# Optimization experiments

Hardware: AMD Instinct MI355X
Metric: run time of the kernel (lower is better)

Reference implementation:

```python
import jax, jax.numpy as jnp
import numpy as np

B, N, M, D = 64, 197, 65, 768


def setup_inputs() -> dict:
    key = jax.random.key(0)
    k1, k2, k3 = jax.random.split(key, 3)
    image = jax.random.normal(k1, (B, N, D), dtype=jnp.float32)
    text = jax.random.normal(k2, (B, M, D), dtype=jnp.float32)
    pm = jax.random.randint(k3, (B, M), 0, 2).astype(jnp.int32)
    pm = pm.at[:, :2].set(0)  # CLS + first real token always valid
    logit_scale = jnp.ones((), dtype=jnp.float32)
    return {"image": image, "text": text, "padding_masks": pm, "logit_scale": logit_scale}


def _ce_with_diag_labels(logits):
    # F.cross_entropy(logits, arange(B)): mean of -log_softmax diag
    return -jnp.mean(jnp.diagonal(jax.nn.log_softmax(logits, axis=-1)))


def reference(image, text, padding_masks, logit_scale):
    # include_cls_token=False: original computes full [B,B,N,M] then slices
    # [:, :, 1:, 1:]; we compute the sliced tokens directly (same math).
    img = image[:, 1:, :]                   # [B, N-1, D]
    txt = text[:, 1:, :]                    # [B, M-1, D]
    pm = padding_masks[:, 1:].astype(bool)  # [B, M-1] True = padded

    # sim[i,j,n,m] = logit_scale * <img_i,n , txt_j,m>
    sim = logit_scale * jnp.einsum('ind,jmd->ijnm', img, txt)  # [B,B,N-1,M-1]

    # Original masks with NaN along mask of batch-row i (broadcast over j,n).
    # logits_per_image: nan_to_num(-inf) -> max over m -> mean over n
    sim_img = jnp.where(pm[:, None, None, :], -jnp.inf, sim)
    logits_per_image = jnp.mean(jnp.max(sim_img, axis=3), axis=2)  # [B,B]

    # logits_per_text: max over n (NaN cols stay NaN) -> nanmean over m.
    # Equivalent masked mean over valid m (mask constant along n).
    max_n = jnp.max(sim, axis=2)                         # [B,B,M-1]
    valid = ~pm                                          # [B,M-1]
    cnt = jnp.sum(valid, axis=1).astype(sim.dtype)       # [B]
    logits_per_text = jnp.sum(
        jnp.where(valid[:, None, :], max_n, 0.0), axis=2
    ) / cnt[:, None]                                     # [B,B]

    loss = 0.5 * (_ce_with_diag_labels(logits_per_image)
                  + _ce_with_diag_labels(logits_per_text))
    targets = jnp.arange(logits_per_image.shape[0], dtype=jnp.int32)
    return loss, logits_per_image, logits_per_text, targets
```

## Files before the change

### kernel.cpp

```cpp
#include <hip/hip_runtime.h>

typedef _Float16 half8 __attribute__((ext_vector_type(8)));
typedef float floatx4 __attribute__((ext_vector_type(4)));
typedef float float4v __attribute__((ext_vector_type(4)));

#define AUNITS (64 * 13 * 24 * 64)
#define TUNITS (64 * 4 * 24 * 64)
#define A_HALFS ((size_t)AUNITS * 8)
#define BJ_HALFS (24 * 4 * 64 * 8)
#define AI_HALFS (13 * 24 * 512)

__device__ __forceinline__ void gl_lds16(const _Float16* g, _Float16* l) {
  __builtin_amdgcn_global_load_lds(
      (const __attribute__((address_space(1))) unsigned int*)g,
      (__attribute__((address_space(3))) unsigned int*)l, 16, 0, 0);
}

__global__ __launch_bounds__(256) void repack(const float* __restrict__ img,
                                              const float* __restrict__ txt,
                                              _Float16* __restrict__ Apk,
                                              _Float16* __restrict__ Bpk) {
  int gid = blockIdx.x * 256 + threadIdx.x;
  const float* src;
  _Float16* dst;
  if (gid < AUNITS) {
    int l = gid & 63, g = gid >> 6;
    int s = g % 24; g /= 24;
    int tau = g % 13; int i = g / 13;
    int n = tau * 16 + (l & 15); if (n > 195) n = 195;
    src = img + (size_t)i * 197 * 768 + (size_t)(n + 1) * 768 + s * 32 + (l >> 4) * 8;
    dst = Apk + (size_t)gid * 8;
  } else {
    int u = gid - AUNITS;
    int l = u & 63, g = u >> 6;
    int ct = g & 3; g >>= 2;
    int s = g % 24; int j = g / 24;
    int m = ct * 16 + (l & 15);
    src = txt + (size_t)j * 65 * 768 + (size_t)(m + 1) * 768 + s * 32 + (l >> 4) * 8;
    dst = Bpk + (size_t)u * 8;
  }
  float4v v0 = *(const float4v*)src;
  float4v v1 = *(const float4v*)(src + 4);
  half8 h;
  h[0] = (_Float16)v0[0]; h[1] = (_Float16)v0[1]; h[2] = (_Float16)v0[2]; h[3] = (_Float16)v0[3];
  h[4] = (_Float16)v1[0]; h[5] = (_Float16)v1[1]; h[6] = (_Float16)v1[2]; h[7] = (_Float16)v1[3];
  *(half8*)dst = h;
}

__global__ __launch_bounds__(256, 4) void sim_kernel(const _Float16* __restrict__ Apk,
                                                     const _Float16* __restrict__ Bpk,
                                                     const int* __restrict__ pm,
                                                     const float* __restrict__ ls,
                                                     float* __restrict__ lpi,
                                                     float* __restrict__ lpt) {
  __shared__ _Float16 Bsh[16384];

  const int j = blockIdx.x, i = blockIdx.y;
  const int tid = threadIdx.x;
  const int wave = tid >> 6, lane = tid & 63;
  const int r16 = lane & 15;
  const int lane8 = lane * 8;

  const _Float16* Ai = Apk + (size_t)i * AI_HALFS;
  const _Float16* pA[4];
  pA[0] = Ai + (size_t)(wave)     * 24 * 512 + lane8;
  pA[1] = Ai + (size_t)(wave + 4) * 24 * 512 + lane8;
  pA[2] = Ai + (size_t)(wave + 8) * 24 * 512 + lane8;
  pA[3] = Ai + (size_t)12         * 24 * 512 + lane8;
  const _Float16* Bg = Bpk + (size_t)j * BJ_HALFS;

  auto stage = [&](int cc) {
    const int buf = cc & 1;
#pragma unroll
    for (int r4 = 0; r4 < 4; ++r4) {
      int rr = wave * 4 + r4;
      gl_lds16(Bg + (size_t)(4 * cc) * 2048 + rr * 512 + lane8,
               Bsh + buf * 8192 + rr * 512);
    }
  };

  stage(0);
  __builtin_amdgcn_sched_barrier(0);
  half8 af[4];
#pragma unroll
  for (int t = 0; t < 4; ++t) af[t] = *(const half8*)(pA[t]);
  __builtin_amdgcn_sched_barrier(0);
  asm volatile("s_waitcnt vmcnt(4)" ::: "memory");
  __builtin_amdgcn_s_barrier();
  __builtin_amdgcn_sched_barrier(0);

  floatx4 acc[3][4];
  floatx4 acc12 = (floatx4){0.f, 0.f, 0.f, 0.f};
#pragma unroll
  for (int t = 0; t < 3; ++t)
#pragma unroll
    for (int cc = 0; cc < 4; ++cc)
      acc[t][cc] = (floatx4){0.f, 0.f, 0.f, 0.f};

#pragma unroll
  for (int c = 0; c < 6; ++c) {
#pragma unroll
    for (int sc = 0; sc < 4; ++sc) {
      const int s = c * 4 + sc;

      if (sc == 0 && c > 0) {
        asm volatile("s_waitcnt vmcnt(16)" ::: "memory");
        __builtin_amdgcn_s_barrier();
        __builtin_amdgcn_sched_barrier(0);
      }

      const int base = (c & 1) * 8192 + sc * 2048 + lane8;
      half8 b[4];
#pragma unroll
      for (int cc = 0; cc < 4; ++cc) {
        int ct = (wave + cc) & 3;
        b[cc] = *(const half8*)(Bsh + base + ct * 512);
      }

      if (sc == 0 && c < 5) {
        stage(c + 1);
        __builtin_amdgcn_sched_barrier(0);
      }

      __builtin_amdgcn_s_setprio(1);
#pragma unroll
      for (int cc = 0; cc < 4; ++cc) {
        acc[0][cc] = __builtin_amdgcn_mfma_f32_16x16x32_f16(af[0], b[cc], acc[0][cc], 0, 0, 0);
        acc[1][cc] = __builtin_amdgcn_mfma_f32_16x16x32_f16(af[1], b[cc], acc[1][cc], 0, 0, 0);
        acc[2][cc] = __builtin_amdgcn_mfma_f32_16x16x32_f16(af[2], b[cc], acc[2][cc], 0, 0, 0);
      }
      acc12 = __builtin_amdgcn_mfma_f32_16x16x32_f16(af[3], b[0], acc12, 0, 0, 0);
      __builtin_amdgcn_s_setprio(0);

      if (s < 23) {
#pragma unroll
        for (int t = 0; t < 4; ++t) af[t] = *(const half8*)(pA[t] + (s + 1) * 512);
      }
      __builtin_amdgcn_sched_barrier(0);
    }
  }

  const float sgl = ls[0];
  bool msk[4];
  int colc[4];
#pragma unroll
  for (int cc = 0; cc < 4; ++cc) {
    colc[cc] = ((wave + cc) & 3) * 16 + r16;
    msk[cc] = pm[i * 65 + 1 + colc[cc]] != 0;
  }

  float rowsum = 0.f;
  float cmv[4];
#pragma unroll
  for (int t = 0; t < 3; ++t) {
#pragma unroll
    for (int r = 0; r < 4; ++r) {
      float rm = -__builtin_inff();
#pragma unroll
      for (int cc = 0; cc < 4; ++cc) {
        float v = acc[t][cc][r] * sgl;
        rm = fmaxf(rm, msk[cc] ? -__builtin_inff() : v);
      }
#pragma unroll
      for (int off = 1; off < 16; off <<= 1)
        rm = fmaxf(rm, __shfl_xor(rm, off, 64));
      rowsum += rm;
    }
  }
#pragma unroll
  for (int off = 1; off < 64; off <<= 1) rowsum += __shfl_xor(rowsum, off, 64);

#pragma unroll
  for (int cc = 0; cc < 4; ++cc) {
    float cm = -__builtin_inff();
#pragma unroll
    for (int t = 0; t < 3; ++t)
#pragma unroll
      for (int r = 0; r < 4; ++r)
        cm = fmaxf(cm, acc[t][cc][r] * sgl);
    cm = fmaxf(cm, __shfl_xor(cm, 16, 64));
    cm = fmaxf(cm, __shfl_xor(cm, 32, 64));
    cmv[cc] = cm;
  }

  __syncthreads();
  float* colmaxS = (float*)Bsh;
  float* t12S    = (float*)Bsh + 256;
  float* wsumS   = (float*)Bsh + 512;

  if (lane == 0) wsumS[wave] = rowsum;
  if (lane < 16) {
#pragma unroll
    for (int cc = 0; cc < 4; ++cc) colmaxS[wave * 64 + colc[cc]] = cmv[cc];
#pragma unroll
    for (int r = 0; r < 4; ++r) t12S[r * 64 + wave * 16 + r16] = acc12[r] * sgl;
  }
  __syncthreads();

  if (tid < 64) {
    const int col = lane;
    bool valid = pm[i * 65 + 1 + col] == 0;
    float t0 = t12S[col], t1 = t12S[64 + col], t2 = t12S[128 + col], t3 = t12S[192 + col];
    float v = fmaxf(fmaxf(colmaxS[col], colmaxS[64 + col]),
                    fmaxf(colmaxS[128 + col], colmaxS[192 + col]));
    v = fmaxf(v, fmaxf(fmaxf(t0, t1), fmaxf(t2, t3)));
    float contrib = valid ? v : 0.f;
    float cntv = valid ? 1.f : 0.f;
    float rs0 = valid ? t0 : -__builtin_inff();
    float rs1 = valid ? t1 : -__builtin_inff();
    float rs2 = valid ? t2 : -__builtin_inff();
    float rs3 = valid ? t3 : -__builtin_inff();
#pragma unroll
    for (int off = 1; off < 64; off <<= 1) {
      contrib += __shfl_xor(contrib, off, 64);
      cntv += __shfl_xor(cntv, off, 64);
      rs0 = fmaxf(rs0, __shfl_xor(rs0, off, 64));
      rs1 = fmaxf(rs1, __shfl_xor(rs1, off, 64));
      rs2 = fmaxf(rs2, __shfl_xor(rs2, off, 64));
      rs3 = fmaxf(rs3, __shfl_xor(rs3, off, 64));
    }
    if (lane == 0) {
      lpt[i * 64 + j] = contrib / cntv;
      float wtot = wsumS[0] + wsumS[1] + wsumS[2] + wsumS[3];
      lpi[i * 64 + j] = (wtot * 0.0625f + rs0 + rs1 + rs2 + rs3) / 196.f;
    }
  }
}

__global__ __launch_bounds__(128) void ce_kernel(float* __restrict__ out) {
  __shared__ float part[2];
  const int tid = threadIdx.x;
  const int t = tid & 63;
  const float* src = (tid < 64) ? (out + 1) : (out + 1 + 4096);

  float mx = -__builtin_inff();
#pragma unroll
  for (int jj = 0; jj < 64; ++jj) mx = fmaxf(mx, src[t * 64 + jj]);
  float se = 0.f;
#pragma unroll
  for (int jj = 0; jj < 64; ++jj) se += __expf(src[t * 64 + jj] - mx);
  float v = (mx + __logf(se)) - src[t * 64 + t];

#pragma unroll
  for (int off = 1; off < 64; off <<= 1) v += __shfl_xor(v, off, 64);
  if (t == 0) part[tid >> 6] = v;
  __syncthreads();
  if (tid == 0) out[0] = 0.5f * (part[0] + part[1]) / 64.f;
  if (tid < 64) out[1 + 8192 + tid] = (float)tid;
}

extern "C" void kernel_launch(void* const* d_in, const int* in_sizes, int n_in,
                              void* d_out, int out_size, void* d_ws, size_t ws_size,
                              hipStream_t stream) {
  const float* image = (const float*)d_in[0];
  const float* text  = (const float*)d_in[1];
  const int*   pm    = (const int*)d_in[2];
  const float* ls    = (const float*)d_in[3];
  float* out = (float*)d_out;

  _Float16* Apk = (_Float16*)d_ws;
  _Float16* Bpk = Apk + A_HALFS;

  repack<<<(AUNITS + TUNITS) / 256, 256, 0, stream>>>(image, text, Apk, Bpk);

  dim3 grid(64, 64);
  sim_kernel<<<grid, 256, 0, stream>>>(Apk, Bpk, pm, ls, out + 1, out + 1 + 4096);
  ce_kernel<<<1, 128, 0, stream>>>(out);
}
```

Measured before the change: 184.0 us.

## Double-buffer LDS B-fragment reads in registers and relax occupancy bound

Prefetches the next sub-chunk's B fragments from shared memory into a second register buffer while the MFMAs for the current sub-chunk run, so LDS read latency is hidden behind the matrix ops. The launch bound drops from 4 to 3 blocks per CU to give room for the extra registers. The setprio hints and some sched_barriers are removed. This trades occupancy and scheduler fencing for software pipelining.

```diff
diff --git a/kernel.cpp b/kernel.cpp
--- a/kernel.cpp
+++ b/kernel.cpp
@@ -47,7 +47,7 @@
   *(half8*)dst = h;
 }
 
-__global__ __launch_bounds__(256, 4) void sim_kernel(const _Float16* __restrict__ Apk,
+__global__ __launch_bounds__(256, 3) void sim_kernel(const _Float16* __restrict__ Apk,
                                                      const _Float16* __restrict__ Bpk,
                                                      const int* __restrict__ pm,
                                                      const float* __restrict__ ls,
@@ -97,40 +97,47 @@
     for (int cc = 0; cc < 4; ++cc)
       acc[t][cc] = (floatx4){0.f, 0.f, 0.f, 0.f};
 
+  half8 b[2][4];
+
 #pragma unroll
   for (int c = 0; c < 6; ++c) {
+    if (c > 0) {
+      asm volatile("s_waitcnt vmcnt(16)" ::: "memory");
+      __builtin_amdgcn_s_barrier();
+      __builtin_amdgcn_sched_barrier(0);
+    }
+
+    {
+      const int base = (c & 1) * 8192 + lane8;
+#pragma unroll
+      for (int cc = 0; cc < 4; ++cc) {
+        int ct = (wave + cc) & 3;
+        b[0][cc] = *(const half8*)(Bsh + base + ct * 512);
+      }
+    }
+    if (c < 5) stage(c + 1);
+
 #pragma unroll
     for (int sc = 0; sc < 4; ++sc) {
       const int s = c * 4 + sc;
-
-      if (sc == 0 && c > 0) {
-        asm volatile("s_waitcnt vmcnt(16)" ::: "memory");
-        __builtin_amdgcn_s_barrier();
-        __builtin_amdgcn_sched_barrier(0);
-      }
-
-      const int base = (c & 1) * 8192 + sc * 2048 + lane8;
-      half8 b[4];
+      const int cur = sc & 1;
+
+      if (sc < 3) {
+        const int nbase = (c & 1) * 8192 + (sc + 1) * 2048 + lane8;
+#pragma unroll
+        for (int cc = 0; cc < 4; ++cc) {
+          int ct = (wave + cc) & 3;
+          b[cur ^ 1][cc] = *(const half8*)(Bsh + nbase + ct * 512);
+        }
+      }
+
 #pragma unroll
       for (int cc = 0; cc < 4; ++cc) {
-        int ct = (wave + cc) & 3;
-        b[cc] = *(const half8*)(Bsh + base + ct * 512);
-      }
-
-      if (sc == 0 && c < 5) {
-        stage(c + 1);
-        __builtin_amdgcn_sched_barrier(0);
-      }
-
-      __builtin_amdgcn_s_setprio(1);
-#pragma unroll
-      for (int cc = 0; cc < 4; ++cc) {
-        acc[0][cc] = __builtin_amdgcn_mfma_f32_16x16x32_f16(af[0], b[cc], acc[0][cc], 0, 0, 0);
-        acc[1][cc] = __builtin_amdgcn_mfma_f32_16x16x32_f16(af[1], b[cc], acc[1][cc], 0, 0, 0);
-        acc[2][cc] = __builtin_amdgcn_mfma_f32_16x16x32_f16(af[2], b[cc], acc[2][cc], 0, 0, 0);
-      }
-      acc12 = __builtin_amdgcn_mfma_f32_16x16x32_f16(af[3], b[0], acc12, 0, 0, 0);
-      __builtin_amdgcn_s_setprio(0);
+        acc[0][cc] = __builtin_amdgcn_mfma_f32_16x16x32_f16(af[0], b[cur][cc], acc[0][cc], 0, 0, 0);
+        acc[1][cc] = __builtin_amdgcn_mfma_f32_16x16x32_f16(af[1], b[cur][cc], acc[1][cc], 0, 0, 0);
+        acc[2][cc] = __builtin_amdgcn_mfma_f32_16x16x32_f16(af[2], b[cur][cc], acc[2][cc], 0, 0, 0);
+      }
+      acc12 = __builtin_amdgcn_mfma_f32_16x16x32_f16(af[3], b[cur][0], acc12, 0, 0, 0);
 
       if (s < 23) {
 #pragma unroll
```

Result: no change. 184.3 us (+0.2%).

## Fuse fp32-to-fp16 repack into similarity kernel, loading raw fp32 inputs directly

Applied to the files above, without the earlier changes.

Removes the separate repack kernel and has the similarity kernel read fp32 image and text directly, converting to fp16 in registers before the MFMA ops. Text tiles are staged into LDS as fp32 with half the K depth per stage, so there are twice as many pipeline stages. This drops one launch and the write/read round trip of packed fp16 data. In exchange, each block re-reads fp32 data (twice the bytes), does redundant conversions, and launch bounds drop to 3 blocks per CU. Grid axes are swapped so consecutive blocks share the same image row.

```diff
diff --git a/kernel.cpp b/kernel.cpp
--- a/kernel.cpp
+++ b/kernel.cpp
@@ -4,78 +4,56 @@
 typedef float floatx4 __attribute__((ext_vector_type(4)));
 typedef float float4v __attribute__((ext_vector_type(4)));
 
-#define AUNITS (64 * 13 * 24 * 64)
-#define TUNITS (64 * 4 * 24 * 64)
-#define A_HALFS ((size_t)AUNITS * 8)
-#define BJ_HALFS (24 * 4 * 64 * 8)
-#define AI_HALFS (13 * 24 * 512)
-
-__device__ __forceinline__ void gl_lds16(const _Float16* g, _Float16* l) {
+__device__ __forceinline__ void gl_lds16f(const float* g, float* l) {
   __builtin_amdgcn_global_load_lds(
       (const __attribute__((address_space(1))) unsigned int*)g,
       (__attribute__((address_space(3))) unsigned int*)l, 16, 0, 0);
 }
 
-__global__ __launch_bounds__(256) void repack(const float* __restrict__ img,
-                                              const float* __restrict__ txt,
-                                              _Float16* __restrict__ Apk,
-                                              _Float16* __restrict__ Bpk) {
-  int gid = blockIdx.x * 256 + threadIdx.x;
-  const float* src;
-  _Float16* dst;
-  if (gid < AUNITS) {
-    int l = gid & 63, g = gid >> 6;
-    int s = g % 24; g /= 24;
-    int tau = g % 13; int i = g / 13;
-    int n = tau * 16 + (l & 15); if (n > 195) n = 195;
-    src = img + (size_t)i * 197 * 768 + (size_t)(n + 1) * 768 + s * 32 + (l >> 4) * 8;
-    dst = Apk + (size_t)gid * 8;
-  } else {
-    int u = gid - AUNITS;
-    int l = u & 63, g = u >> 6;
-    int ct = g & 3; g >>= 2;
-    int s = g % 24; int j = g / 24;
-    int m = ct * 16 + (l & 15);
-    src = txt + (size_t)j * 65 * 768 + (size_t)(m + 1) * 768 + s * 32 + (l >> 4) * 8;
-    dst = Bpk + (size_t)u * 8;
-  }
-  float4v v0 = *(const float4v*)src;
-  float4v v1 = *(const float4v*)(src + 4);
+__device__ __forceinline__ half8 cvt8(float4v u0, float4v u1) {
   half8 h;
-  h[0] = (_Float16)v0[0]; h[1] = (_Float16)v0[1]; h[2] = (_Float16)v0[2]; h[3] = (_Float16)v0[3];
-  h[4] = (_Float16)v1[0]; h[5] = (_Float16)v1[1]; h[6] = (_Float16)v1[2]; h[7] = (_Float16)v1[3];
-  *(half8*)dst = h;
-}
-
-__global__ __launch_bounds__(256, 4) void sim_kernel(const _Float16* __restrict__ Apk,
-                                                     const _Float16* __restrict__ Bpk,
+  h[0] = (_Float16)u0[0]; h[1] = (_Float16)u0[1];
+  h[2] = (_Float16)u0[2]; h[3] = (_Float16)u0[3];
+  h[4] = (_Float16)u1[0]; h[5] = (_Float16)u1[1];
+  h[6] = (_Float16)u1[2]; h[7] = (_Float16)u1[3];
+  return h;
+}
+
+__global__ __launch_bounds__(256, 3) void sim_kernel(const float* __restrict__ img,
+                                                     const float* __restrict__ txt,
                                                      const int* __restrict__ pm,
                                                      const float* __restrict__ ls,
                                                      float* __restrict__ lpi,
                                                      float* __restrict__ lpt) {
-  __shared__ _Float16 Bsh[16384];
-
-  const int j = blockIdx.x, i = blockIdx.y;
+  __shared__ float Bsh[8192];
+
+  const int i = blockIdx.x, j = blockIdx.y;
   const int tid = threadIdx.x;
   const int wave = tid >> 6, lane = tid & 63;
   const int r16 = lane & 15;
-  const int lane8 = lane * 8;
-
-  const _Float16* Ai = Apk + (size_t)i * AI_HALFS;
-  const _Float16* pA[4];
-  pA[0] = Ai + (size_t)(wave)     * 24 * 512 + lane8;
-  pA[1] = Ai + (size_t)(wave + 4) * 24 * 512 + lane8;
-  pA[2] = Ai + (size_t)(wave + 8) * 24 * 512 + lane8;
-  pA[3] = Ai + (size_t)12         * 24 * 512 + lane8;
-  const _Float16* Bg = Bpk + (size_t)j * BJ_HALFS;
+
+  const float* A1 = img + (size_t)i * 197 * 768 + 768;
+  const float* pAf[4];
+  {
+    const int tls[4] = {wave, wave + 4, wave + 8, 12};
+#pragma unroll
+    for (int t = 0; t < 4; ++t) {
+      int r = tls[t] * 16 + r16;
+      if (r > 195) r = 195;
+      pAf[t] = A1 + (size_t)r * 768 + (lane >> 4) * 8;
+    }
+  }
+  const float* Bsrc = txt + (size_t)j * 65 * 768 + 768
+                      + (size_t)r16 * 768 + (lane >> 4) * 8;
 
   auto stage = [&](int cc) {
     const int buf = cc & 1;
 #pragma unroll
-    for (int r4 = 0; r4 < 4; ++r4) {
-      int rr = wave * 4 + r4;
-      gl_lds16(Bg + (size_t)(4 * cc) * 2048 + rr * 512 + lane8,
-               Bsh + buf * 8192 + rr * 512);
+    for (int k = 0; k < 4; ++k) {
+      int p = wave * 4 + k;
+      int sc = p >> 3, ct = (p >> 1) & 3, h = p & 1;
+      gl_lds16f(Bsrc + (size_t)(ct * 16) * 768 + (2 * cc + sc) * 32 + h * 4,
+                Bsh + buf * 4096 + p * 256);
     }
   };
 
@@ -83,7 +61,11 @@
   __builtin_amdgcn_sched_barrier(0);
   half8 af[4];
 #pragma unroll
-  for (int t = 0; t < 4; ++t) af[t] = *(const half8*)(pA[t]);
+  for (int t = 0; t < 4; ++t) {
+    float4v u0 = *(const float4v*)(pAf[t]);
+    float4v u1 = *(const float4v*)(pAf[t] + 4);
+    af[t] = cvt8(u0, u1);
+  }
   __builtin_amdgcn_sched_barrier(0);
   asm volatile("s_waitcnt vmcnt(4)" ::: "memory");
   __builtin_amdgcn_s_barrier();
@@ -98,26 +80,28 @@
       acc[t][cc] = (floatx4){0.f, 0.f, 0.f, 0.f};
 
 #pragma unroll
-  for (int c = 0; c < 6; ++c) {
-#pragma unroll
-    for (int sc = 0; sc < 4; ++sc) {
-      const int s = c * 4 + sc;
-
-      if (sc == 0 && c > 0) {
-        asm volatile("s_waitcnt vmcnt(16)" ::: "memory");
-        __builtin_amdgcn_s_barrier();
-        __builtin_amdgcn_sched_barrier(0);
-      }
-
-      const int base = (c & 1) * 8192 + sc * 2048 + lane8;
+  for (int c = 0; c < 12; ++c) {
+    if (c > 0) {
+      asm volatile("s_waitcnt vmcnt(16)" ::: "memory");
+      __builtin_amdgcn_s_barrier();
+      __builtin_amdgcn_sched_barrier(0);
+    }
+
+#pragma unroll
+    for (int sc = 0; sc < 2; ++sc) {
+      const int s = c * 2 + sc;
+
+      const int base = (c & 1) * 4096 + sc * 2048 + lane * 4;
       half8 b[4];
 #pragma unroll
       for (int cc = 0; cc < 4; ++cc) {
         int ct = (wave + cc) & 3;
-        b[cc] = *(const half8*)(Bsh + base + ct * 512);
-      }
-
-      if (sc == 0 && c < 5) {
+        float4v f0 = *(const float4v*)(Bsh + base + ct * 512);
+        float4v f1 = *(const float4v*)(Bsh + base + ct * 512 + 256);
+        b[cc] = cvt8(f0, f1);
+      }
+
+      if (sc == 0 && c < 11) {
         stage(c + 1);
         __builtin_amdgcn_sched_barrier(0);
       }
@@ -134,7 +118,11 @@
 
       if (s < 23) {
 #pragma unroll
-        for (int t = 0; t < 4; ++t) af[t] = *(const half8*)(pA[t] + (s + 1) * 512);
+        for (int t = 0; t < 4; ++t) {
+          float4v u0 = *(const float4v*)(pAf[t] + (s + 1) * 32);
+          float4v u1 = *(const float4v*)(pAf[t] + (s + 1) * 32 + 4);
+          af[t] = cvt8(u0, u1);
+        }
       }
       __builtin_amdgcn_sched_barrier(0);
     }
@@ -184,9 +172,9 @@
   }
 
   __syncthreads();
-  float* colmaxS = (float*)Bsh;
-  float* t12S    = (float*)Bsh + 256;
-  float* wsumS   = (float*)Bsh + 512;
+  float* colmaxS = Bsh;
+  float* t12S    = Bsh + 256;
+  float* wsumS   = Bsh + 512;
 
   if (lane == 0) wsumS[wave] = rowsum;
   if (lane < 16) {
@@ -258,12 +246,7 @@
   const float* ls    = (const float*)d_in[3];
   float* out = (float*)d_out;
 
-  _Float16* Apk = (_Float16*)d_ws;
-  _Float16* Bpk = Apk + A_HALFS;
-
-  repack<<<(AUNITS + TUNITS) / 256, 256, 0, stream>>>(image, text, Apk, Bpk);
-
   dim3 grid(64, 64);
-  sim_kernel<<<grid, 256, 0, stream>>>(Apk, Bpk, pm, ls, out + 1, out + 1 + 4096);
+  sim_kernel<<<grid, 256, 0, stream>>>(image, text, pm, ls, out + 1, out + 1 + 4096);
   ce_kernel<<<1, 128, 0, stream>>>(out);
 }
```

Measured after the change: 460.4 us. 2.5x slower.
